# Kernel optimization log

Hardware: AMD Instinct MI355X
Metric: run time of the kernel (lower is better)

## Reference

```python
import jax, jax.numpy as jnp
import numpy as np

DIM = 2048
N_HEADS = 16
N_KV_HEADS = 4
HEAD_DIM = DIM // N_HEADS  # 128
N_REP = N_HEADS // N_KV_HEADS  # 4
SEQ = 2048
BATCH = 2


def apply_rope(x, cos, sin):
    # x: [b, s, h, d]; cos/sin: [s, d//2]
    xr = x[..., 0::2]
    xi = x[..., 1::2]
    c = cos[None, :, None, :]
    s = sin[None, :, None, :]
    out_r = xr * c - xi * s
    out_i = xr * s + xi * c
    # interleave back: stack on last axis then flatten
    out = jnp.stack([out_r, out_i], axis=-1)
    return out.reshape(x.shape)


def setup_inputs() -> dict:
    key = jax.random.key(0)
    ks = jax.random.split(key, 7)
    x = jax.random.normal(ks[0], (BATCH, SEQ, DIM), dtype=jnp.float32)
    # realistic rotary tables
    inv_freq = 1.0 / (10000.0 ** (np.arange(0, HEAD_DIM, 2, dtype=np.float32) / HEAD_DIM))
    t = np.arange(SEQ, dtype=np.float32)
    freqs = np.outer(t, inv_freq)  # [S, d//2]
    freqs_cos = jnp.asarray(np.cos(freqs))
    freqs_sin = jnp.asarray(np.sin(freqs))
    sc = 0.02
    Wq = jax.random.normal(ks[1], (DIM, N_HEADS * HEAD_DIM), dtype=jnp.float32) * sc
    Wk = jax.random.normal(ks[2], (DIM, N_KV_HEADS * HEAD_DIM), dtype=jnp.float32) * sc
    Wv = jax.random.normal(ks[3], (DIM, N_KV_HEADS * HEAD_DIM), dtype=jnp.float32) * sc
    Wo = jax.random.normal(ks[4], (N_HEADS * HEAD_DIM, DIM), dtype=jnp.float32) * sc
    return {"x": x, "freqs_cos": freqs_cos, "freqs_sin": freqs_sin,
            "Wq": Wq, "Wk": Wk, "Wv": Wv, "Wo": Wo}


def reference(x, freqs_cos, freqs_sin, Wq, Wk, Wv, Wo):
    b, s, _ = x.shape
    xq = (x @ Wq).reshape(b, s, N_HEADS, HEAD_DIM)
    xk = (x @ Wk).reshape(b, s, N_KV_HEADS, HEAD_DIM)
    xv = (x @ Wv).reshape(b, s, N_KV_HEADS, HEAD_DIM)
    xq = apply_rope(xq, freqs_cos, freqs_sin)
    xk = apply_rope(xk, freqs_cos, freqs_sin)
    # GQA attention without materializing repeated KV:
    # group query heads as [b, g, r, s, d] with g=N_KV_HEADS, r=N_REP
    q = xq.reshape(b, s, N_KV_HEADS, N_REP, HEAD_DIM)
    scale = 1.0 / jnp.sqrt(jnp.float32(HEAD_DIM))
    scores = jnp.einsum('bqgrd,bkgd->bgrqk', q, xk) * scale  # [b,g,r,s,s]
    causal = jnp.tril(jnp.ones((s, s), dtype=bool))
    scores = jnp.where(causal[None, None, None], scores, jnp.finfo(scores.dtype).min)
    probs = jax.nn.softmax(scores, axis=-1)
    out = jnp.einsum('bgrqk,bkgd->bqgrd', probs, xv)  # [b,s,g,r,d]
    out = out.reshape(b, s, N_HEADS * HEAD_DIM)
    return out @ Wo
```

## Files before the change

kernel.cpp:

```cpp
#include <hip/hip_runtime.h>
#include <stdint.h>
#include <stddef.h>

constexpr int BATCH = 2;
constexpr int SEQ   = 2048;
constexpr int EMB   = 2048;
constexpr int HEADS = 16;
constexpr int GQA   = 4;
constexpr int HDIM  = 128;
constexpr int NQKV  = 3072;
constexpr int VOFF  = 2560;
constexpr int MROWS = BATCH * SEQ;

typedef _Float16 half8  __attribute__((ext_vector_type(8)));
typedef _Float16 half4v __attribute__((ext_vector_type(4)));
typedef float    floatx4 __attribute__((ext_vector_type(4)));

__device__ __forceinline__ void st_c(float* p, float v)    { *p = v; }
__device__ __forceinline__ void st_c(_Float16* p, float v) { *p = (_Float16)v; }

__device__ __forceinline__ void gld16(const _Float16* g, _Float16* l) {
    __builtin_amdgcn_global_load_lds(
        (const __attribute__((address_space(1))) void*)g,
        (__attribute__((address_space(3))) void*)l, 16, 0, 0);
}

__global__ void cast_x_kernel(const float* __restrict__ x, _Float16* __restrict__ xh) {
    int i = (blockIdx.x * 256 + threadIdx.x) * 4;
    float4 v = *(const float4*)(x + i);
    half4v h;
    h[0] = (_Float16)v.x; h[1] = (_Float16)v.y; h[2] = (_Float16)v.z; h[3] = (_Float16)v.w;
    *(half4v*)(xh + i) = h;
}

__global__ void transpose_cast(const float* __restrict__ in, _Float16* __restrict__ out,
                               int R, int C) {
    __shared__ float tile[32][33];
    int cb = blockIdx.x * 32, rb = blockIdx.y * 32;
    int tx = threadIdx.x, ty = threadIdx.y;
    #pragma unroll
    for (int j = 0; j < 32; j += 8)
        tile[ty + j][tx] = in[(size_t)(rb + ty + j) * C + (cb + tx)];
    __syncthreads();
    #pragma unroll
    for (int j = 0; j < 32; j += 8)
        out[(size_t)(cb + ty + j) * R + (rb + tx)] = (_Float16)tile[tx][ty + j];
}

template <typename CT, bool ROPE>
__global__ __launch_bounds__(256) void gemm_bt(const _Float16* __restrict__ A,
                                               const _Float16* __restrict__ Bt,
                                               CT* __restrict__ C,
                                               int M, int N, int K,
                                               const float* __restrict__ fc,
                                               const float* __restrict__ fs) {
    __shared__ _Float16 As[128 * 32];
    __shared__ _Float16 Bs[128 * 32];
    const int tid  = threadIdx.x;
    const int bm   = blockIdx.y * 128, bn = blockIdx.x * 128;
    const int lane = tid & 63, wid = tid >> 6;
    const int wr   = wid >> 1, wc = wid & 1;
    const int qd   = lane >> 4, m15 = lane & 15;

    const int srow = lane >> 2;
    const int scol = (lane & 3) * 8;
    const _Float16* Ag = A  + (size_t)(bm + wid * 16 + srow) * K + scol;
    const _Float16* Bg = Bt + (size_t)(bn + wid * 16 + srow) * K + scol;
    const size_t rowskip = (size_t)64 * K;
    _Float16* AsW = As + wid * 16 * 32;
    _Float16* BsW = Bs + wid * 16 * 32;

    const _Float16* AsR = As + (wr * 64 + m15) * 32 + qd * 8;
    const _Float16* BsR = Bs + (wc * 64 + m15) * 32 + qd * 8;

    floatx4 acc[4][4] = {};

    for (int k0 = 0; k0 < K; k0 += 32) {
        gld16(Ag + k0,           AsW);
        gld16(Ag + rowskip + k0, AsW + 64 * 32);
        gld16(Bg + k0,           BsW);
        gld16(Bg + rowskip + k0, BsW + 64 * 32);
        __syncthreads();
        half8 af[4], bf[4];
        #pragma unroll
        for (int i = 0; i < 4; i++) af[i] = *(const half8*)(AsR + i * 16 * 32);
        #pragma unroll
        for (int i = 0; i < 4; i++) bf[i] = *(const half8*)(BsR + i * 16 * 32);
        #pragma unroll
        for (int mi = 0; mi < 4; mi++)
            #pragma unroll
            for (int ni = 0; ni < 4; ni++)
                acc[mi][ni] = __builtin_amdgcn_mfma_f32_16x16x32_f16(af[mi], bf[ni], acc[mi][ni], 0, 0, 0);
        __syncthreads();
    }

    #pragma unroll
    for (int mi = 0; mi < 4; mi++)
        #pragma unroll
        for (int ni = 0; ni < 4; ni++)
            #pragma unroll
            for (int r = 0; r < 4; r++) {
                int row = bm + wr * 64 + mi * 16 + qd * 4 + r;
                int col = bn + wc * 64 + ni * 16 + m15;
                float v = acc[mi][ni][r];
                if (ROPE && col < VOFF) {
                    int si = row & (SEQ - 1);
                    int fi = (col >> 1) & 63;
                    float c  = fc[si * 64 + fi];
                    float sn = fs[si * 64 + fi];
                    float other = __shfl_xor(v, 1, 64);
                    v = (m15 & 1) ? (v * c + other * sn) : (v * c - other * sn);
                }
                st_c(&C[(size_t)row * N + col], v);
            }
}

__global__ void transpose_v(const _Float16* __restrict__ qkv, _Float16* __restrict__ vt) {
    __shared__ _Float16 tile[32][33];
    int sb = blockIdx.x * 32, db = blockIdx.y * 32;
    int bg = blockIdx.z;
    int tx = threadIdx.x, ty = threadIdx.y;
    const _Float16* src = qkv + (size_t)(bg >> 2) * SEQ * NQKV + VOFF + (bg & 3) * HDIM;
    #pragma unroll
    for (int j = 0; j < 32; j += 8)
        tile[ty + j][tx] = src[(size_t)(sb + ty + j) * NQKV + db + tx];
    __syncthreads();
    _Float16* dst = vt + (size_t)bg * HDIM * SEQ;
    #pragma unroll
    for (int j = 0; j < 32; j += 8)
        dst[(size_t)(db + ty + j) * SEQ + sb + tx] = tile[tx][ty + j];
}

__global__ __launch_bounds__(512, 2) void flash_attn(const _Float16* __restrict__ qkv,
                                                     const _Float16* __restrict__ vt,
                                                     _Float16* __restrict__ ob) {
    const int bx   = blockIdx.x;
    const int g    = blockIdx.y;
    const int b    = blockIdx.z;
    const int tid  = threadIdx.x;
    const int lane = tid & 63, wid = tid >> 6;
    const int h    = g * 4 + (wid & 3);
    const int su   = wid >> 2;
    const int qd   = lane >> 4, m15 = lane & 15;

    __shared__ _Float16 Ks[2][64 * 128];
    __shared__ _Float16 Vs[2][128 * 64];
    __shared__ _Float16 Ps[8][16 * 64];

    const _Float16* kg = qkv + (size_t)(b * SEQ) * NQKV + EMB + g * HDIM;
    const _Float16* vg = vt + (size_t)(b * GQA + g) * HDIM * SEQ;
    _Float16* pw = Ps[wid];

    const int kl = lane >> 4, kc16 = lane & 15;
    const int vl = lane >> 3, vc8  = lane & 7;
    const _Float16* kgp[2]; const _Float16* vgp[2];
    int ksoff[2], vsoff[2];
    #pragma unroll
    for (int j = 0; j < 2; j++) {
        int t = wid * 2 + j;
        int kr = t * 4 + kl;
        kgp[j] = kg + (size_t)kr * NQKV + ((kc16 ^ (kr & 15)) * 8);
        ksoff[j] = t * 512;
        int vr = t * 8 + vl;
        vgp[j] = vg + (size_t)vr * SEQ + ((vc8 ^ (vr & 7)) * 8);
        vsoff[j] = t * 512;
    }

    half8 ones;
    #pragma unroll
    for (int i = 0; i < 8; i++) ones[i] = (_Float16)1.0f;
    const _Float16 qsc = (_Float16)(0.08838834764831845f * 1.44269504088896341f);

    for (int ph = 0; ph < 2; ++ph) {
        const int sidx   = ph ? bx : 63 - bx;
        const int q0     = sidx * 32;
        const int ktLast = sidx >> 1;

        __syncthreads();
        #pragma unroll
        for (int j = 0; j < 2; j++) gld16(kgp[j], &Ks[0][ksoff[j]]);
        #pragma unroll
        for (int j = 0; j < 2; j++) gld16(vgp[j], &Vs[0][vsoff[j]]);

        half8 qf[4];
        {
            const _Float16* qb = qkv + (size_t)(b * SEQ + q0 + su * 16 + m15) * NQKV + h * HDIM + qd * 8;
            #pragma unroll
            for (int kc = 0; kc < 4; kc++) {
                half8 q = *(const half8*)(qb + kc * 32);
                #pragma unroll
                for (int i = 0; i < 8; i++) q[i] = (_Float16)(q[i] * qsc);
                qf[kc] = q;
            }
        }

        floatx4 o[9] = {};

        for (int kt = 0; kt <= ktLast; ++kt) {
            const int cur = kt & 1;
            __syncthreads();
            if (kt < ktLast) {
                const int nb = cur ^ 1;
                const size_t ko = (size_t)(kt + 1) * 64;
                #pragma unroll
                for (int j = 0; j < 2; j++) gld16(kgp[j] + ko * NQKV, &Ks[nb][ksoff[j]]);
                #pragma unroll
                for (int j = 0; j < 2; j++) gld16(vgp[j] + ko, &Vs[nb][vsoff[j]]);
            }
            const _Float16* ksb = Ks[cur];
            const _Float16* vsb = Vs[cur];

            floatx4 sa[4] = {};
            __builtin_amdgcn_s_setprio(1);
            #pragma unroll
            for (int nt = 0; nt < 4; ++nt) {
                const int kr = nt * 16 + m15;
                #pragma unroll
                for (int kc = 0; kc < 4; ++kc) {
                    half8 kf = *(const half8*)(&ksb[kr * 128 + (((kc * 4 + qd) ^ (kr & 15)) * 8)]);
                    sa[nt] = __builtin_amdgcn_mfma_f32_16x16x32_f16(qf[kc], kf, sa[nt], 0, 0, 0);
                }
            }
            __builtin_amdgcn_s_setprio(0);

            const bool diag = (kt == ktLast);
            const int  k0   = kt * 64;
            #pragma unroll
            for (int r = 0; r < 4; r++) {
                const int prow = qd * 4 + r;
                const int rowg = q0 + su * 16 + prow;
                #pragma unroll
                for (int nt = 0; nt < 4; nt++) {
                    float p = __builtin_exp2f(sa[nt][r]);
                    if (diag && (k0 + nt * 16 + m15 > rowg)) p = 0.f;
                    int chunk = (nt * 2 + (m15 >> 3)) ^ (prow & 7);
                    pw[prow * 64 + chunk * 8 + (m15 & 7)] = (_Float16)p;
                }
            }

            half8 pf[2];
            #pragma unroll
            for (int kc = 0; kc < 2; kc++)
                pf[kc] = *(const half8*)(&pw[m15 * 64 + (((kc * 4 + qd) ^ (m15 & 7)) * 8)]);

            __builtin_amdgcn_s_setprio(1);
            #pragma unroll
            for (int dt = 0; dt < 8; dt++) {
                const int vr = dt * 16 + m15;
                #pragma unroll
                for (int kc = 0; kc < 2; kc++) {
                    half8 vf = *(const half8*)(&vsb[vr * 64 + (((kc * 4 + qd) ^ (vr & 7)) * 8)]);
                    o[dt] = __builtin_amdgcn_mfma_f32_16x16x32_f16(pf[kc], vf, o[dt], 0, 0, 0);
                }
            }
            o[8] = __builtin_amdgcn_mfma_f32_16x16x32_f16(pf[0], ones, o[8], 0, 0, 0);
            o[8] = __builtin_amdgcn_mfma_f32_16x16x32_f16(pf[1], ones, o[8], 0, 0, 0);
            __builtin_amdgcn_s_setprio(0);
        }

        float linv[4];
        #pragma unroll
        for (int r = 0; r < 4; r++) linv[r] = 1.0f / o[8][r];
        _Float16* od = ob + (size_t)(b * SEQ + q0 + su * 16) * EMB + h * HDIM;
        #pragma unroll
        for (int dt = 0; dt < 8; dt++)
            #pragma unroll
            for (int r = 0; r < 4; r++)
                od[(size_t)(qd * 4 + r) * EMB + dt * 16 + m15] = (_Float16)(o[dt][r] * linv[r]);
    }
}

extern "C" void kernel_launch(void* const* d_in, const int* in_sizes, int n_in,
                              void* d_out, int out_size, void* d_ws, size_t ws_size,
                              hipStream_t stream) {
    (void)in_sizes; (void)n_in; (void)out_size; (void)ws_size;
    const float* x  = (const float*)d_in[0];
    const float* fc = (const float*)d_in[1];
    const float* fs = (const float*)d_in[2];
    const float* Wq = (const float*)d_in[3];
    const float* Wk = (const float*)d_in[4];
    const float* Wv = (const float*)d_in[5];
    const float* Wo = (const float*)d_in[6];
    float* out = (float*)d_out;

    _Float16* Xb   = (_Float16*)d_ws;
    _Float16* Wqkv = Xb   + (size_t)MROWS * EMB;
    _Float16* WoT  = Wqkv + (size_t)NQKV * EMB;
    _Float16* C1   = WoT  + (size_t)EMB * EMB;
    _Float16* Vt   = Wqkv;
    _Float16* Ob   = Xb;

    dim3 tb(32, 8);
    cast_x_kernel<<<MROWS * EMB / 1024, 256, 0, stream>>>(x, Xb);
    transpose_cast<<<dim3(EMB / 32, EMB / 32), tb, 0, stream>>>(Wq, Wqkv, EMB, EMB);
    transpose_cast<<<dim3(512 / 32, EMB / 32), tb, 0, stream>>>(Wk, Wqkv + (size_t)EMB * EMB, EMB, 512);
    transpose_cast<<<dim3(512 / 32, EMB / 32), tb, 0, stream>>>(Wv, Wqkv + (size_t)VOFF * EMB, EMB, 512);
    transpose_cast<<<dim3(EMB / 32, EMB / 32), tb, 0, stream>>>(Wo, WoT, EMB, EMB);

    gemm_bt<_Float16, true><<<dim3(NQKV / 128, MROWS / 128), 256, 0, stream>>>(
        Xb, Wqkv, C1, MROWS, NQKV, EMB, fc, fs);
    transpose_v<<<dim3(SEQ / 32, HDIM / 32, BATCH * GQA), tb, 0, stream>>>(C1, Vt);
    flash_attn<<<dim3(32, GQA, BATCH), 512, 0, stream>>>(C1, Vt, Ob);
    gemm_bt<float, false><<<dim3(EMB / 128, MROWS / 128), 256, 0, stream>>>(
        Ob, WoT, out, MROWS, EMB, EMB, nullptr, nullptr);
}
```

Before: 339.7 us.

## Double-buffer LDS tiles in GEMM to overlap global loads with MFMA

Splits the A and B shared-memory tiles into two buffers and issues the direct-to-LDS global loads for the next K-slice before computing on the current one. The first slice is loaded before the loop, and the trailing barrier is dropped, leaving one barrier per iteration. The aim is to hide global memory latency behind MFMA work and cut synchronisation. It doubles LDS use per block, which can reduce occupancy, and the compiler may still insert conservative waits that limit the overlap.

```diff
diff --git a/kernel.cpp b/kernel.cpp
--- a/kernel.cpp
+++ b/kernel.cpp
@@ -54,8 +54,8 @@
                                                int M, int N, int K,
                                                const float* __restrict__ fc,
                                                const float* __restrict__ fs) {
-    __shared__ _Float16 As[128 * 32];
-    __shared__ _Float16 Bs[128 * 32];
+    __shared__ _Float16 As[2][128 * 32];
+    __shared__ _Float16 Bs[2][128 * 32];
     const int tid  = threadIdx.x;
     const int bm   = blockIdx.y * 128, bn = blockIdx.x * 128;
     const int lane = tid & 63, wid = tid >> 6;
@@ -67,20 +67,30 @@
     const _Float16* Ag = A  + (size_t)(bm + wid * 16 + srow) * K + scol;
     const _Float16* Bg = Bt + (size_t)(bn + wid * 16 + srow) * K + scol;
     const size_t rowskip = (size_t)64 * K;
-    _Float16* AsW = As + wid * 16 * 32;
-    _Float16* BsW = Bs + wid * 16 * 32;
-
-    const _Float16* AsR = As + (wr * 64 + m15) * 32 + qd * 8;
-    const _Float16* BsR = Bs + (wc * 64 + m15) * 32 + qd * 8;
+    const int woff = wid * 16 * 32;
+
+    gld16(Ag,           &As[0][woff]);
+    gld16(Ag + rowskip, &As[0][woff + 64 * 32]);
+    gld16(Bg,           &Bs[0][woff]);
+    gld16(Bg + rowskip, &Bs[0][woff + 64 * 32]);
 
     floatx4 acc[4][4] = {};
-
-    for (int k0 = 0; k0 < K; k0 += 32) {
-        gld16(Ag + k0,           AsW);
-        gld16(Ag + rowskip + k0, AsW + 64 * 32);
-        gld16(Bg + k0,           BsW);
-        gld16(Bg + rowskip + k0, BsW + 64 * 32);
+    const int nk = K >> 5;
+
+    for (int kt = 0; kt < nk; ++kt) {
+        const int cur = kt & 1;
         __syncthreads();
+        if (kt + 1 < nk) {
+            const int ko = (kt + 1) * 32;
+            _Float16* aw = &As[cur ^ 1][woff];
+            _Float16* bw = &Bs[cur ^ 1][woff];
+            gld16(Ag + ko,           aw);
+            gld16(Ag + rowskip + ko, aw + 64 * 32);
+            gld16(Bg + ko,           bw);
+            gld16(Bg + rowskip + ko, bw + 64 * 32);
+        }
+        const _Float16* AsR = &As[cur][(wr * 64 + m15) * 32 + qd * 8];
+        const _Float16* BsR = &Bs[cur][(wc * 64 + m15) * 32 + qd * 8];
         half8 af[4], bf[4];
         #pragma unroll
         for (int i = 0; i < 4; i++) af[i] = *(const half8*)(AsR + i * 16 * 32);
@@ -91,7 +101,6 @@
             #pragma unroll
             for (int ni = 0; ni < 4; ni++)
                 acc[mi][ni] = __builtin_amdgcn_mfma_f32_16x16x32_f16(af[mi], bf[ni], acc[mi][ni], 0, 0, 0);
-        __syncthreads();
     }
 
     #pragma unroll
```

Result: faster. 322.6 us (-5.1%).

## Rewrite GEMMs as 8-wave multi-stage pipelined kernels with swizzled LDS

Applied to the files above, without the earlier changes.

Replaces the 256-thread 128x128 single-buffered GEMM with a 512-thread kernel using larger tiles (256x256 for QKV, 128x256 for the output projection). It adds a four-slot LDS ring with explicit vmcnt waits so global-to-LDS loads overlap MFMA work, and XOR-swizzles LDS chunks to cut bank conflicts. s_setprio is raised around the MFMA block. The aim is to hide memory latency and raise data reuse per block. The cost is fewer blocks in flight (QKV grid becomes 12x16), which can leave CUs idle, plus more fragile hand-written synchronisation.

```diff
diff --git a/kernel.cpp b/kernel.cpp
--- a/kernel.cpp
+++ b/kernel.cpp
@@ -25,6 +25,15 @@
         (__attribute__((address_space(3))) void*)l, 16, 0, 0);
 }
 
+template <int N>
+__device__ __forceinline__ void waitvm() {
+    if constexpr (N == 8)      asm volatile("s_waitcnt vmcnt(8)" ::: "memory");
+    else if constexpr (N == 6) asm volatile("s_waitcnt vmcnt(6)" ::: "memory");
+    else if constexpr (N == 4) asm volatile("s_waitcnt vmcnt(4)" ::: "memory");
+    else if constexpr (N == 3) asm volatile("s_waitcnt vmcnt(3)" ::: "memory");
+    else                       asm volatile("s_waitcnt vmcnt(0)" ::: "memory");
+}
+
 __global__ void cast_x_kernel(const float* __restrict__ x, _Float16* __restrict__ xh) {
     int i = (blockIdx.x * 256 + threadIdx.x) * 4;
     float4 v = *(const float4*)(x + i);
@@ -47,61 +56,89 @@
         out[(size_t)(cb + ty + j) * R + (rb + tx)] = (_Float16)tile[tx][ty + j];
 }
 
-template <typename CT, bool ROPE>
-__global__ __launch_bounds__(256) void gemm_bt(const _Float16* __restrict__ A,
-                                               const _Float16* __restrict__ Bt,
-                                               CT* __restrict__ C,
-                                               int M, int N, int K,
-                                               const float* __restrict__ fc,
-                                               const float* __restrict__ fs) {
-    __shared__ _Float16 As[128 * 32];
-    __shared__ _Float16 Bs[128 * 32];
+template <int BM, int BN, int MF, int NF, typename CT, bool ROPE>
+__global__ __launch_bounds__(512, 2) void gemm_8p(const _Float16* __restrict__ A,
+                                                  const _Float16* __restrict__ Bt,
+                                                  CT* __restrict__ C,
+                                                  int M, int N, int K,
+                                                  const float* __restrict__ fc,
+                                                  const float* __restrict__ fs) {
+    constexpr int GROUP = BM / 128 + BN / 128;
+    __shared__ _Float16 As[4 * BM * 32];
+    __shared__ _Float16 Bs[4 * BN * 32];
     const int tid  = threadIdx.x;
-    const int bm   = blockIdx.y * 128, bn = blockIdx.x * 128;
+    const int bm   = blockIdx.y * BM, bn = blockIdx.x * BN;
     const int lane = tid & 63, wid = tid >> 6;
-    const int wr   = wid >> 1, wc = wid & 1;
+    const int wr   = wid >> 2, wc = wid & 3;
     const int qd   = lane >> 4, m15 = lane & 15;
 
-    const int srow = lane >> 2;
-    const int scol = (lane & 3) * 8;
-    const _Float16* Ag = A  + (size_t)(bm + wid * 16 + srow) * K + scol;
-    const _Float16* Bg = Bt + (size_t)(bn + wid * 16 + srow) * K + scol;
-    const size_t rowskip = (size_t)64 * K;
-    _Float16* AsW = As + wid * 16 * 32;
-    _Float16* BsW = Bs + wid * 16 * 32;
-
-    const _Float16* AsR = As + (wr * 64 + m15) * 32 + qd * 8;
-    const _Float16* BsR = Bs + (wc * 64 + m15) * 32 + qd * 8;
-
-    floatx4 acc[4][4] = {};
-
-    for (int k0 = 0; k0 < K; k0 += 32) {
-        gld16(Ag + k0,           AsW);
-        gld16(Ag + rowskip + k0, AsW + 64 * 32);
-        gld16(Bg + k0,           BsW);
-        gld16(Bg + rowskip + k0, BsW + 64 * 32);
-        __syncthreads();
-        half8 af[4], bf[4];
-        #pragma unroll
-        for (int i = 0; i < 4; i++) af[i] = *(const half8*)(AsR + i * 16 * 32);
-        #pragma unroll
-        for (int i = 0; i < 4; i++) bf[i] = *(const half8*)(BsR + i * 16 * 32);
-        #pragma unroll
-        for (int mi = 0; mi < 4; mi++)
-            #pragma unroll
-            for (int ni = 0; ni < 4; ni++)
+    const int srow   = lane >> 2;
+    const int schunk = (lane & 3) ^ ((lane >> 3) & 3);
+    const _Float16* Ag = A  + (size_t)(bm + wid * 16 + srow) * K + schunk * 8;
+    const _Float16* Bg = Bt + (size_t)(bn + wid * 16 + srow) * K + schunk * 8;
+
+    floatx4 acc[MF][NF] = {};
+
+    auto STAGE = [&](int tt, int kk, int ss) {
+        const int koff = tt * 64 + kk * 32;
+        _Float16* aw = As + (ss * 2 + kk) * (BM * 32) + wid * 16 * 32;
+        gld16(Ag + koff, aw);
+        if constexpr (BM == 256) gld16(Ag + (size_t)128 * K + koff, aw + 128 * 32);
+        _Float16* bw = Bs + (ss * 2 + kk) * (BN * 32) + wid * 16 * 32;
+        gld16(Bg + koff, bw);
+        if constexpr (BN == 256) gld16(Bg + (size_t)128 * K + koff, bw + 128 * 32);
+    };
+
+    const int rsw = (qd ^ ((m15 >> 1) & 3)) * 8;
+
+    auto COMPUTE = [&](int ss, int kk) {
+        const _Float16* ab = As + (ss * 2 + kk) * (BM * 32);
+        const _Float16* bb = Bs + (ss * 2 + kk) * (BN * 32);
+        half8 bf[NF], af[MF];
+        #pragma unroll
+        for (int i = 0; i < NF; i++)
+            bf[i] = *(const half8*)(bb + (wc * (BN / 4) + i * 16 + m15) * 32 + rsw);
+        #pragma unroll
+        for (int i = 0; i < MF; i++)
+            af[i] = *(const half8*)(ab + (wr * (BM / 2) + i * 16 + m15) * 32 + rsw);
+        __builtin_amdgcn_s_setprio(1);
+        #pragma unroll
+        for (int mi = 0; mi < MF; mi++)
+            #pragma unroll
+            for (int ni = 0; ni < NF; ni++)
                 acc[mi][ni] = __builtin_amdgcn_mfma_f32_16x16x32_f16(af[mi], bf[ni], acc[mi][ni], 0, 0, 0);
-        __syncthreads();
+        __builtin_amdgcn_s_setprio(0);
+    };
+
+    const int nt = K >> 6;
+    STAGE(0, 0, 0);
+    STAGE(0, 1, 0);
+    STAGE(1, 0, 1);
+
+    for (int t = 0; t < nt; ++t) {
+        const int s = t & 1;
+        if (t + 1 < nt) waitvm<2 * GROUP>();
+        else            waitvm<GROUP>();
+        __builtin_amdgcn_s_barrier();
+        if (t + 1 < nt) STAGE(t + 1, 1, s ^ 1);
+        COMPUTE(s, 0);
+        __builtin_amdgcn_s_barrier();
+        if (t + 1 < nt) waitvm<2 * GROUP>();
+        else            waitvm<0>();
+        __builtin_amdgcn_s_barrier();
+        if (t + 2 < nt) STAGE(t + 2, 0, s);
+        COMPUTE(s, 1);
+        __builtin_amdgcn_s_barrier();
     }
 
     #pragma unroll
-    for (int mi = 0; mi < 4; mi++)
-        #pragma unroll
-        for (int ni = 0; ni < 4; ni++)
+    for (int mi = 0; mi < MF; mi++)
+        #pragma unroll
+        for (int ni = 0; ni < NF; ni++)
             #pragma unroll
             for (int r = 0; r < 4; r++) {
-                int row = bm + wr * 64 + mi * 16 + qd * 4 + r;
-                int col = bn + wc * 64 + ni * 16 + m15;
+                int row = bm + wr * (BM / 2) + mi * 16 + qd * 4 + r;
+                int col = bn + wc * (BN / 4) + ni * 16 + m15;
                 float v = acc[mi][ni][r];
                 if (ROPE && col < VOFF) {
                     int si = row & (SEQ - 1);
@@ -297,10 +334,10 @@
     transpose_cast<<<dim3(512 / 32, EMB / 32), tb, 0, stream>>>(Wv, Wqkv + (size_t)VOFF * EMB, EMB, 512);
     transpose_cast<<<dim3(EMB / 32, EMB / 32), tb, 0, stream>>>(Wo, WoT, EMB, EMB);
 
-    gemm_bt<_Float16, true><<<dim3(NQKV / 128, MROWS / 128), 256, 0, stream>>>(
+    gemm_8p<256, 256, 8, 4, _Float16, true><<<dim3(NQKV / 256, MROWS / 256), 512, 0, stream>>>(
         Xb, Wqkv, C1, MROWS, NQKV, EMB, fc, fs);
     transpose_v<<<dim3(SEQ / 32, HDIM / 32, BATCH * GQA), tb, 0, stream>>>(C1, Vt);
     flash_attn<<<dim3(32, GQA, BATCH), 512, 0, stream>>>(C1, Vt, Ob);
-    gemm_bt<float, false><<<dim3(EMB / 128, MROWS / 128), 256, 0, stream>>>(
+    gemm_8p<128, 256, 4, 4, float, false><<<dim3(EMB / 256, MROWS / 128), 512, 0, stream>>>(
         Ob, WoT, out, MROWS, EMB, EMB, nullptr, nullptr);
 }
```

New measurement: 356.4 us. 4.9% more time.

## Replace GEMMs with double-buffered, swizzled, larger-tile 8-wave pipelined kernels

Applied to the files above, without the earlier changes.

Replaces the simple single-buffered 128x128 GEMM with two specialised kernels: a 256x192-tile QKV projection with fused RoPE and a 128x256-tile output projection. Both use 512 threads, K-step 64, double-buffered LDS with XOR swizzling, staged async global-to-LDS loads interleaved between MFMA phases, and s_setprio around the MFMA blocks. The aim is to hide global-memory latency, avoid LDS bank conflicts and raise arithmetic intensity per tile. It increases LDS use and register pressure, and the hand-placed vmcnt waits are fragile. The QKV grid also shrinks to 16x16 blocks, which may leave some CUs underfilled.

```diff
diff --git a/kernel.cpp b/kernel.cpp
--- a/kernel.cpp
+++ b/kernel.cpp
@@ -47,63 +47,128 @@
         out[(size_t)(cb + ty + j) * R + (rb + tx)] = (_Float16)tile[tx][ty + j];
 }
 
-template <typename CT, bool ROPE>
-__global__ __launch_bounds__(256) void gemm_bt(const _Float16* __restrict__ A,
-                                               const _Float16* __restrict__ Bt,
-                                               CT* __restrict__ C,
-                                               int M, int N, int K,
-                                               const float* __restrict__ fc,
-                                               const float* __restrict__ fs) {
-    __shared__ _Float16 As[128 * 32];
-    __shared__ _Float16 Bs[128 * 32];
+
+__global__ __launch_bounds__(512, 2) void gemm_qkv(const _Float16* __restrict__ A,
+                                                   const _Float16* __restrict__ Bt,
+                                                   _Float16* __restrict__ C,
+                                                   int M, int N, int K,
+                                                   const float* __restrict__ fc,
+                                                   const float* __restrict__ fs) {
+    constexpr int BM = 256, BN = 192;
+    __shared__ _Float16 As[2][BM * 64];
+    __shared__ _Float16 Bs[2][BN * 64];
     const int tid  = threadIdx.x;
-    const int bm   = blockIdx.y * 128, bn = blockIdx.x * 128;
+    const int bm   = blockIdx.y * BM, bn = blockIdx.x * BN;
     const int lane = tid & 63, wid = tid >> 6;
-    const int wr   = wid >> 1, wc = wid & 1;
+    const int wr   = wid >> 2, wc = wid & 3;
     const int qd   = lane >> 4, m15 = lane & 15;
-
-    const int srow = lane >> 2;
-    const int scol = (lane & 3) * 8;
-    const _Float16* Ag = A  + (size_t)(bm + wid * 16 + srow) * K + scol;
-    const _Float16* Bg = Bt + (size_t)(bn + wid * 16 + srow) * K + scol;
-    const size_t rowskip = (size_t)64 * K;
-    _Float16* AsW = As + wid * 16 * 32;
-    _Float16* BsW = Bs + wid * 16 * 32;
-
-    const _Float16* AsR = As + (wr * 64 + m15) * 32 + qd * 8;
-    const _Float16* BsR = Bs + (wc * 64 + m15) * 32 + qd * 8;
-
-    floatx4 acc[4][4] = {};
-
-    for (int k0 = 0; k0 < K; k0 += 32) {
-        gld16(Ag + k0,           AsW);
-        gld16(Ag + rowskip + k0, AsW + 64 * 32);
-        gld16(Bg + k0,           BsW);
-        gld16(Bg + rowskip + k0, BsW + 64 * 32);
-        __syncthreads();
-        half8 af[4], bf[4];
-        #pragma unroll
-        for (int i = 0; i < 4; i++) af[i] = *(const half8*)(AsR + i * 16 * 32);
-        #pragma unroll
-        for (int i = 0; i < 4; i++) bf[i] = *(const half8*)(BsR + i * 16 * 32);
-        #pragma unroll
-        for (int mi = 0; mi < 4; mi++)
-            #pragma unroll
-            for (int ni = 0; ni < 4; ni++)
-                acc[mi][ni] = __builtin_amdgcn_mfma_f32_16x16x32_f16(af[mi], bf[ni], acc[mi][ni], 0, 0, 0);
-        __syncthreads();
+    const int l8   = lane >> 3, c8 = lane & 7;
+    const int schunk = c8 ^ (l8 & 7);
+
+    const _Float16* Ag = A  + (size_t)(bm + wid * 8 + l8) * K + schunk * 8;
+    const _Float16* Bg = Bt + (size_t)(bn + wid * 8 + l8) * K + schunk * 8;
+    _Float16* AsW = &As[0][0] + wid * 8 * 64;
+    _Float16* BsW = &Bs[0][0] + wid * 8 * 64;
+
+    auto stA = [&](int s, int R0, int k) { gld16(Ag + (size_t)R0 * K + k, AsW + s * (BM * 64) + R0 * 64); };
+    auto stB = [&](int s, int R0, int k) { gld16(Bg + (size_t)R0 * K + k, BsW + s * (BN * 64) + R0 * 64); };
+
+    floatx4 acc[8][3] = {};
+    const int nt = K >> 6;
+    const int rswz = m15 & 7;
+
+    stA(0, 0, 0); stA(0, 64, 0); stA(0, 128, 0); stA(0, 192, 0);
+    stB(0, 0, 0); stB(0, 64, 0); stB(0, 128, 0);
+    stB(1, 0, 64); stB(1, 64, 64); stB(1, 128, 64);
+    asm volatile("s_waitcnt vmcnt(3)" ::: "memory");
+    __builtin_amdgcn_s_barrier();
+
+    for (int u = 0; u < nt; ++u) {
+        const int s  = u & 1;
+        const int kn = (u + 1) * 64, kn2 = (u + 2) * 64;
+        const _Float16* Ab = &As[s][0];
+        const _Float16* Bb = &Bs[s][0];
+        half8 af[4][2], bf01[2][2], bf2[2];
+
+        #pragma unroll
+        for (int mi = 0; mi < 4; mi++)
+            #pragma unroll
+            for (int k2 = 0; k2 < 2; k2++)
+                af[mi][k2] = *(const half8*)(Ab + (wr * 128 + mi * 16 + m15) * 64 + (((k2 * 4 + qd) ^ rswz) * 8));
+        #pragma unroll
+        for (int ni = 0; ni < 2; ni++)
+            #pragma unroll
+            for (int k2 = 0; k2 < 2; k2++)
+                bf01[ni][k2] = *(const half8*)(Bb + (wc * 48 + ni * 16 + m15) * 64 + (((k2 * 4 + qd) ^ rswz) * 8));
+        if (u + 1 < nt) { stA(s ^ 1, 0, kn); stA(s ^ 1, 128, kn); }
+        __builtin_amdgcn_s_barrier();
+        __builtin_amdgcn_s_setprio(1);
+        #pragma unroll
+        for (int mi = 0; mi < 4; mi++)
+            #pragma unroll
+            for (int ni = 0; ni < 2; ni++)
+                #pragma unroll
+                for (int k2 = 0; k2 < 2; k2++)
+                    acc[mi][ni] = __builtin_amdgcn_mfma_f32_16x16x32_f16(af[mi][k2], bf01[ni][k2], acc[mi][ni], 0, 0, 0);
+        __builtin_amdgcn_s_setprio(0);
+        __builtin_amdgcn_s_barrier();
+
+        #pragma unroll
+        for (int k2 = 0; k2 < 2; k2++)
+            bf2[k2] = *(const half8*)(Bb + (wc * 48 + 2 * 16 + m15) * 64 + (((k2 * 4 + qd) ^ rswz) * 8));
+        if (u + 1 < nt) { stA(s ^ 1, 64, kn); stA(s ^ 1, 192, kn); }
+        __builtin_amdgcn_s_barrier();
+        __builtin_amdgcn_s_setprio(1);
+        #pragma unroll
+        for (int mi = 0; mi < 4; mi++)
+            #pragma unroll
+            for (int k2 = 0; k2 < 2; k2++)
+                acc[mi][2] = __builtin_amdgcn_mfma_f32_16x16x32_f16(af[mi][k2], bf2[k2], acc[mi][2], 0, 0, 0);
+        __builtin_amdgcn_s_setprio(0);
+        __builtin_amdgcn_s_barrier();
+
+        #pragma unroll
+        for (int mi = 0; mi < 4; mi++)
+            #pragma unroll
+            for (int k2 = 0; k2 < 2; k2++)
+                af[mi][k2] = *(const half8*)(Ab + (wr * 128 + 64 + mi * 16 + m15) * 64 + (((k2 * 4 + qd) ^ rswz) * 8));
+        if (u + 2 < nt) { stB(s, 0, kn2); stB(s, 64, kn2); }
+        __builtin_amdgcn_s_barrier();
+        __builtin_amdgcn_s_setprio(1);
+        #pragma unroll
+        for (int mi = 0; mi < 4; mi++)
+            #pragma unroll
+            for (int k2 = 0; k2 < 2; k2++)
+                acc[4 + mi][2] = __builtin_amdgcn_mfma_f32_16x16x32_f16(af[mi][k2], bf2[k2], acc[4 + mi][2], 0, 0, 0);
+        __builtin_amdgcn_s_setprio(0);
+        __builtin_amdgcn_s_barrier();
+
+        if (u + 2 < nt) stB(s, 128, kn2);
+        if (u + 2 < nt)      { asm volatile("s_waitcnt vmcnt(3)" ::: "memory"); }
+        else if (u + 1 < nt) { asm volatile("s_waitcnt vmcnt(0)" ::: "memory"); }
+        __builtin_amdgcn_s_barrier();
+        __builtin_amdgcn_s_setprio(1);
+        #pragma unroll
+        for (int mi = 0; mi < 4; mi++)
+            #pragma unroll
+            for (int ni = 0; ni < 2; ni++)
+                #pragma unroll
+                for (int k2 = 0; k2 < 2; k2++)
+                    acc[4 + mi][ni] = __builtin_amdgcn_mfma_f32_16x16x32_f16(af[mi][k2], bf01[ni][k2], acc[4 + mi][ni], 0, 0, 0);
+        __builtin_amdgcn_s_setprio(0);
+        __builtin_amdgcn_s_barrier();
     }
 
     #pragma unroll
-    for (int mi = 0; mi < 4; mi++)
-        #pragma unroll
-        for (int ni = 0; ni < 4; ni++)
+    for (int ai = 0; ai < 8; ai++)
+        #pragma unroll
+        for (int ni = 0; ni < 3; ni++)
             #pragma unroll
             for (int r = 0; r < 4; r++) {
-                int row = bm + wr * 64 + mi * 16 + qd * 4 + r;
-                int col = bn + wc * 64 + ni * 16 + m15;
-                float v = acc[mi][ni][r];
-                if (ROPE && col < VOFF) {
+                int row = bm + wr * 128 + ai * 16 + qd * 4 + r;
+                int col = bn + wc * 48 + ni * 16 + m15;
+                float v = acc[ai][ni][r];
+                if (col < VOFF) {
                     int si = row & (SEQ - 1);
                     int fi = (col >> 1) & 63;
                     float c  = fc[si * 64 + fi];
@@ -111,7 +176,134 @@
                     float other = __shfl_xor(v, 1, 64);
                     v = (m15 & 1) ? (v * c + other * sn) : (v * c - other * sn);
                 }
-                st_c(&C[(size_t)row * N + col], v);
+                C[(size_t)row * N + col] = (_Float16)v;
+            }
+}
+
+__global__ __launch_bounds__(512, 2) void gemm_out(const _Float16* __restrict__ A,
+                                                   const _Float16* __restrict__ Bt,
+                                                   float* __restrict__ C,
+                                                   int M, int N, int K) {
+    constexpr int BM = 128, BN = 256;
+    __shared__ _Float16 As[2][BM * 64];
+    __shared__ _Float16 Bs[2][BN * 64];
+    const int tid  = threadIdx.x;
+    const int bm   = blockIdx.y * BM, bn = blockIdx.x * BN;
+    const int lane = tid & 63, wid = tid >> 6;
+    const int wr   = wid >> 2, wc = wid & 3;
+    const int qd   = lane >> 4, m15 = lane & 15;
+    const int l8   = lane >> 3, c8 = lane & 7;
+    const int schunk = c8 ^ (l8 & 7);
+
+    const _Float16* Ag = A  + (size_t)(bm + wid * 8 + l8) * K + schunk * 8;
+    const _Float16* Bg = Bt + (size_t)(bn + wid * 8 + l8) * K + schunk * 8;
+    _Float16* AsW = &As[0][0] + wid * 8 * 64;
+    _Float16* BsW = &Bs[0][0] + wid * 8 * 64;
+
+    auto stA = [&](int s, int R0, int k) { gld16(Ag + (size_t)R0 * K + k, AsW + s * (BM * 64) + R0 * 64); };
+    auto stB = [&](int s, int R0, int k) { gld16(Bg + (size_t)R0 * K + k, BsW + s * (BN * 64) + R0 * 64); };
+
+    floatx4 acc[4][4] = {};
+    const int nt = K >> 6;
+    const int rswz = m15 & 7;
+
+    stA(0, 0, 0); stA(0, 64, 0);
+    stB(0, 0, 0); stB(0, 64, 0); stB(0, 128, 0); stB(0, 192, 0);
+    stB(1, 128, 64); stB(1, 192, 64);
+    asm volatile("s_waitcnt vmcnt(2)" ::: "memory");
+    __builtin_amdgcn_s_barrier();
+
+    for (int u = 0; u < nt; ++u) {
+        const int s  = u & 1;
+        const int kn = (u + 1) * 64, kn2 = (u + 2) * 64;
+        const _Float16* Ab = &As[s][0];
+        const _Float16* Bb = &Bs[s][0];
+        half8 af[2][2], bf01[2][2], bf23[2][2];
+
+        #pragma unroll
+        for (int mi = 0; mi < 2; mi++)
+            #pragma unroll
+            for (int k2 = 0; k2 < 2; k2++)
+                af[mi][k2] = *(const half8*)(Ab + (wr * 64 + mi * 16 + m15) * 64 + (((k2 * 4 + qd) ^ rswz) * 8));
+        #pragma unroll
+        for (int ni = 0; ni < 2; ni++)
+            #pragma unroll
+            for (int k2 = 0; k2 < 2; k2++)
+                bf01[ni][k2] = *(const half8*)(Bb + (wc * 64 + ni * 16 + m15) * 64 + (((k2 * 4 + qd) ^ rswz) * 8));
+        if (u + 1 < nt) { stA(s ^ 1, 0, kn); stA(s ^ 1, 64, kn); }
+        __builtin_amdgcn_s_barrier();
+        __builtin_amdgcn_s_setprio(1);
+        #pragma unroll
+        for (int mi = 0; mi < 2; mi++)
+            #pragma unroll
+            for (int ni = 0; ni < 2; ni++)
+                #pragma unroll
+                for (int k2 = 0; k2 < 2; k2++)
+                    acc[mi][ni] = __builtin_amdgcn_mfma_f32_16x16x32_f16(af[mi][k2], bf01[ni][k2], acc[mi][ni], 0, 0, 0);
+        __builtin_amdgcn_s_setprio(0);
+        __builtin_amdgcn_s_barrier();
+
+        #pragma unroll
+        for (int ni = 0; ni < 2; ni++)
+            #pragma unroll
+            for (int k2 = 0; k2 < 2; k2++)
+                bf23[ni][k2] = *(const half8*)(Bb + (wc * 64 + (2 + ni) * 16 + m15) * 64 + (((k2 * 4 + qd) ^ rswz) * 8));
+        if (u + 1 < nt) { stB(s ^ 1, 0, kn); stB(s ^ 1, 64, kn); }
+        __builtin_amdgcn_s_barrier();
+        __builtin_amdgcn_s_setprio(1);
+        #pragma unroll
+        for (int mi = 0; mi < 2; mi++)
+            #pragma unroll
+            for (int ni = 0; ni < 2; ni++)
+                #pragma unroll
+                for (int k2 = 0; k2 < 2; k2++)
+                    acc[mi][2 + ni] = __builtin_amdgcn_mfma_f32_16x16x32_f16(af[mi][k2], bf23[ni][k2], acc[mi][2 + ni], 0, 0, 0);
+        __builtin_amdgcn_s_setprio(0);
+        __builtin_amdgcn_s_barrier();
+
+        #pragma unroll
+        for (int mi = 0; mi < 2; mi++)
+            #pragma unroll
+            for (int k2 = 0; k2 < 2; k2++)
+                af[mi][k2] = *(const half8*)(Ab + (wr * 64 + 32 + mi * 16 + m15) * 64 + (((k2 * 4 + qd) ^ rswz) * 8));
+        if (u + 2 < nt) stB(s, 128, kn2);
+        __builtin_amdgcn_s_barrier();
+        __builtin_amdgcn_s_setprio(1);
+        #pragma unroll
+        for (int mi = 0; mi < 2; mi++)
+            #pragma unroll
+            for (int ni = 0; ni < 2; ni++)
+                #pragma unroll
+                for (int k2 = 0; k2 < 2; k2++)
+                    acc[2 + mi][2 + ni] = __builtin_amdgcn_mfma_f32_16x16x32_f16(af[mi][k2], bf23[ni][k2], acc[2 + mi][2 + ni], 0, 0, 0);
+        __builtin_amdgcn_s_setprio(0);
+        __builtin_amdgcn_s_barrier();
+
+        if (u + 2 < nt) stB(s, 192, kn2);
+        if (u + 2 < nt)      { asm volatile("s_waitcnt vmcnt(2)" ::: "memory"); }
+        else if (u + 1 < nt) { asm volatile("s_waitcnt vmcnt(0)" ::: "memory"); }
+        __builtin_amdgcn_s_barrier();
+        __builtin_amdgcn_s_setprio(1);
+        #pragma unroll
+        for (int mi = 0; mi < 2; mi++)
+            #pragma unroll
+            for (int ni = 0; ni < 2; ni++)
+                #pragma unroll
+                for (int k2 = 0; k2 < 2; k2++)
+                    acc[2 + mi][ni] = __builtin_amdgcn_mfma_f32_16x16x32_f16(af[mi][k2], bf01[ni][k2], acc[2 + mi][ni], 0, 0, 0);
+        __builtin_amdgcn_s_setprio(0);
+        __builtin_amdgcn_s_barrier();
+    }
+
+    #pragma unroll
+    for (int ai = 0; ai < 4; ai++)
+        #pragma unroll
+        for (int ni = 0; ni < 4; ni++)
+            #pragma unroll
+            for (int r = 0; r < 4; r++) {
+                int row = bm + wr * 64 + ai * 16 + qd * 4 + r;
+                int col = bn + wc * 64 + ni * 16 + m15;
+                C[(size_t)row * N + col] = acc[ai][ni][r];
             }
 }
 
@@ -297,10 +489,10 @@
     transpose_cast<<<dim3(512 / 32, EMB / 32), tb, 0, stream>>>(Wv, Wqkv + (size_t)VOFF * EMB, EMB, 512);
     transpose_cast<<<dim3(EMB / 32, EMB / 32), tb, 0, stream>>>(Wo, WoT, EMB, EMB);
 
-    gemm_bt<_Float16, true><<<dim3(NQKV / 128, MROWS / 128), 256, 0, stream>>>(
+    gemm_qkv<<<dim3(NQKV / 192, MROWS / 256), 512, 0, stream>>>(
         Xb, Wqkv, C1, MROWS, NQKV, EMB, fc, fs);
     transpose_v<<<dim3(SEQ / 32, HDIM / 32, BATCH * GQA), tb, 0, stream>>>(C1, Vt);
     flash_attn<<<dim3(32, GQA, BATCH), 512, 0, stream>>>(C1, Vt, Ob);
-    gemm_bt<float, false><<<dim3(EMB / 128, MROWS / 128), 256, 0, stream>>>(
-        Ob, WoT, out, MROWS, EMB, EMB, nullptr, nullptr);
-}
+    gemm_out<<<dim3(EMB / 256, MROWS / 128), 512, 0, stream>>>(
+        Ob, WoT, out, MROWS, EMB, EMB);
+}
```

Result: faster. 328.1 us (-3.4%).
